# Kernel tuning notes

Hardware: AMD Instinct MI355X
Metric: run time of the kernel (lower is better)

The kernel has to match this reference:

```python
import jax, jax.numpy as jnp
import numpy as np

B, N, DIM = 8, 8192, 512
H, DH = 8, 64
INNER = H * DH
EPS = 1e-5


def setup_inputs() -> dict:
    key = jax.random.key(0)
    ks = jax.random.split(key, 5)
    x = jax.random.normal(ks[0], (B, N, DIM), dtype=jnp.float32)
    w_qkv = jax.random.normal(ks[1], (DIM, 3 * INNER), dtype=jnp.float32) * (DIM ** -0.5)
    ln_w = jnp.ones((INNER,), dtype=jnp.float32)
    ln_b = jnp.zeros((INNER,), dtype=jnp.float32)
    w_out = jax.random.normal(ks[2], (INNER, DIM), dtype=jnp.float32) * (INNER ** -0.5)
    b_out = jnp.zeros((DIM,), dtype=jnp.float32)
    return {"x": x, "w_qkv": w_qkv, "ln_w": ln_w, "ln_b": ln_b,
            "w_out": w_out, "b_out": b_out}


def _layernorm(x, w, b):
    mu = jnp.mean(x, axis=-1, keepdims=True)
    var = jnp.mean(jnp.square(x - mu), axis=-1, keepdims=True)
    return (x - mu) * jax.lax.rsqrt(var + EPS) * w + b


def reference(x, w_qkv, ln_w, ln_b, w_out, b_out):
    b, n, _ = x.shape
    qkv = x @ w_qkv  # [b, n, 3*inner]
    q, k, v = jnp.split(qkv, 3, axis=-1)
    # b n (h d) -> b h n d
    def heads(t):
        return t.reshape(b, n, H, DH).transpose(0, 2, 1, 3)
    q, k, v = heads(q), heads(k), heads(v)
    q = jax.nn.relu(q)
    k = jax.nn.relu(k)
    kv = jnp.einsum('bhnm,bhnd->bhmd', k, v)   # [b, h, d, d]
    out = jnp.einsum('bhnm,bhmd->bhnd', q, kv)  # [b, h, n, d]
    out = out.transpose(0, 2, 1, 3).reshape(b, n, INNER)
    out = _layernorm(out, ln_w, ln_b)
    return out @ w_out + b_out
```

## Files before the change

kernel.cpp:

```cpp
#include <hip/hip_runtime.h>
#include <stdint.h>

#define B_ 8
#define N_ 8192
#define DIM_ 512
#define H_ 8
#define DH_ 64
#define ROWS (B_*N_)
#define TRIPLE (3*DIM_)
#define EPS_ 1e-5f

typedef __attribute__((ext_vector_type(8))) short short8;
typedef __attribute__((ext_vector_type(4))) float f32x4;
typedef __attribute__((ext_vector_type(4))) float fl4;
typedef __attribute__((ext_vector_type(4))) unsigned short us4;
typedef __attribute__((ext_vector_type(8))) unsigned short us8;

#define AS1 __attribute__((address_space(1)))
#define AS3 __attribute__((address_space(3)))

__device__ __forceinline__ void gld16(const void* g, void* l) {
    __builtin_amdgcn_global_load_lds((const AS1 void*)(uintptr_t)g,
                                     (AS3 void*)(unsigned)(uintptr_t)l, 16, 0, 0);
}

__device__ inline unsigned short f2bf(float f) {
    union { float f; unsigned int u; } x; x.f = f;
    unsigned int r = x.u + 0x7fffu + ((x.u >> 16) & 1u);
    return (unsigned short)(r >> 16);
}
__device__ inline float bf2f(unsigned short b) {
    union { unsigned int u; float f; } x; x.u = ((unsigned int)b) << 16;
    return x.f;
}

__global__ __launch_bounds__(256) void k_cvt(const float* __restrict__ x,
                                             unsigned short* __restrict__ xb) {
    size_t i = ((size_t)blockIdx.x * 256 + threadIdx.x) * 8;
    fl4 a = *(const fl4*)(x + i);
    fl4 b = *(const fl4*)(x + i + 4);
    us8 r;
    r[0] = f2bf(a[0]); r[1] = f2bf(a[1]); r[2] = f2bf(a[2]); r[3] = f2bf(a[3]);
    r[4] = f2bf(b[0]); r[5] = f2bf(b[1]); r[6] = f2bf(b[2]); r[7] = f2bf(b[3]);
    *(us8*)(xb + i) = r;
}

__global__ void k_prep(const float* __restrict__ w_qkv, const float* __restrict__ w_out,
                       unsigned short* __restrict__ wqkvT, unsigned short* __restrict__ woutT) {
    int idx = blockIdx.x * 256 + threadIdx.x;
    if (idx < TRIPLE * DIM_) {
        int n = idx / DIM_, k = idx - n * DIM_;
        wqkvT[idx] = f2bf(w_qkv[(size_t)k * TRIPLE + n]);
    }
    if (idx < DIM_ * DIM_) {
        int n = idx / DIM_, k = idx - n * DIM_;
        woutT[idx] = f2bf(w_out[(size_t)k * DIM_ + n]);
    }
}

__global__ __launch_bounds__(256) void k_qkv_a(const unsigned short* __restrict__ xb,
        const unsigned short* __restrict__ wT,
        unsigned short* __restrict__ qkv)
{
    __shared__ unsigned short As[128 * 32];
    __shared__ unsigned short Bs[128 * 32];
    int t = threadIdx.x;
    int lane = t & 63, wave = t >> 6;
    int m0 = blockIdx.y * 128;
    int n0 = blockIdx.x * 128;
    int wm = (wave & 1) * 64, wn = (wave >> 1) * 64;
    int lr = lane & 15, kg = (lane >> 4) * 8;
    int srow = lane >> 2;
    int scol = (lane & 3) * 8;

    f32x4 acc[4][4] = {};
    for (int k0 = 0; k0 < DIM_; k0 += 32) {
#pragma unroll
        for (int i = 0; i < 2; ++i) {
            int c = wave * 2 + i;
            int r = c * 16 + srow;
            gld16(xb + (size_t)(m0 + r) * DIM_ + k0 + scol, &As[c * 512]);
            gld16(wT + (size_t)(n0 + r) * DIM_ + k0 + scol, &Bs[c * 512]);
        }
        __syncthreads();
        short8 af[4], bfr[4];
#pragma unroll
        for (int i = 0; i < 4; ++i) af[i]  = *(short8*)&As[(wm + i*16 + lr) * 32 + kg];
#pragma unroll
        for (int j = 0; j < 4; ++j) bfr[j] = *(short8*)&Bs[(wn + j*16 + lr) * 32 + kg];
#pragma unroll
        for (int i = 0; i < 4; ++i)
#pragma unroll
            for (int j = 0; j < 4; ++j)
                acc[i][j] = __builtin_amdgcn_mfma_f32_16x16x32_bf16(af[i], bfr[j], acc[i][j], 0, 0, 0);
        __syncthreads();
    }
#pragma unroll
    for (int i = 0; i < 4; ++i) {
        int row = m0 + wm + i*16 + (lane >> 4) * 4;
#pragma unroll
        for (int j = 0; j < 4; ++j) {
            int col = n0 + wn + j*16 + (lane & 15);
            bool rl = (col < 1024);
#pragma unroll
            for (int r = 0; r < 4; ++r) {
                float v = acc[i][j][r];
                if (rl && v < 0.0f) v = 0.0f;
                qkv[(size_t)(row + r) * TRIPLE + col] = f2bf(v);
            }
        }
    }
}

__global__ __launch_bounds__(256) void k_qkv_f(const float* __restrict__ x,
        const unsigned short* __restrict__ wT,
        unsigned short* __restrict__ qkv)
{
    __shared__ unsigned short As[128][40];
    __shared__ unsigned short Bs[128][40];
    int t = threadIdx.x;
    int lane = t & 63, wave = t >> 6;
    int m0 = blockIdx.y * 128;
    int n0 = blockIdx.x * 128;
    int wm = (wave & 1) * 64, wn = (wave >> 1) * 64;
    int lr = lane & 15, kg = (lane >> 4) * 8;

    f32x4 acc[4][4] = {};
    for (int k0 = 0; k0 < DIM_; k0 += 32) {
#pragma unroll
        for (int i = 0; i < 4; ++i) {
            int c = t + 256 * i;
            int r = c >> 3, c4 = (c & 7) * 4;
            fl4 v = *(const fl4*)(x + (size_t)(m0 + r) * DIM_ + k0 + c4);
            unsigned short* dst = &As[r][c4];
            dst[0] = f2bf(v[0]); dst[1] = f2bf(v[1]); dst[2] = f2bf(v[2]); dst[3] = f2bf(v[3]);
        }
#pragma unroll
        for (int i = 0; i < 2; ++i) {
            int c = t + 256 * i;
            int r = c >> 2, c8 = (c & 3) * 8;
            *(int4*)&Bs[r][c8] = *(const int4*)(wT + (size_t)(n0 + r) * DIM_ + k0 + c8);
        }
        __syncthreads();
        short8 af[4], bfr[4];
#pragma unroll
        for (int i = 0; i < 4; ++i) af[i]  = *(short8*)&As[wm + i*16 + lr][kg];
#pragma unroll
        for (int j = 0; j < 4; ++j) bfr[j] = *(short8*)&Bs[wn + j*16 + lr][kg];
#pragma unroll
        for (int i = 0; i < 4; ++i)
#pragma unroll
            for (int j = 0; j < 4; ++j)
                acc[i][j] = __builtin_amdgcn_mfma_f32_16x16x32_bf16(af[i], bfr[j], acc[i][j], 0, 0, 0);
        __syncthreads();
    }
#pragma unroll
    for (int i = 0; i < 4; ++i) {
        int row = m0 + wm + i*16 + (lane >> 4) * 4;
#pragma unroll
        for (int j = 0; j < 4; ++j) {
            int col = n0 + wn + j*16 + (lane & 15);
            bool rl = (col < 1024);
#pragma unroll
            for (int r = 0; r < 4; ++r) {
                float v = acc[i][j][r];
                if (rl && v < 0.0f) v = 0.0f;
                qkv[(size_t)(row + r) * TRIPLE + col] = f2bf(v);
            }
        }
    }
}

__global__ __launch_bounds__(256) void k_kv(const unsigned short* __restrict__ qkv,
                                            float* __restrict__ kv)
{
    __shared__ unsigned short KT[64][136];
    __shared__ unsigned short VT[64][136];
    __shared__ float red[64 * 64];
    int t = threadIdx.x, lane = t & 63, wave = t >> 6;
    int bh = blockIdx.x;
    int b = bh >> 3, h = bh & 7;
    int chunk = blockIdx.y;
    size_t rowbase = (size_t)b * N_ + (size_t)chunk * 1024;
    int kcol = DIM_ + h * 64;
    int vcol = 2 * DIM_ + h * 64;
    int lr = lane & 15;

    f32x4 acc[4][4] = {};
    for (int tile = 0; tile < 8; ++tile) {
        size_t r0 = rowbase + tile * 128;
#pragma unroll
        for (int i = 0; i < 8; ++i) {
            int c = t + 256 * i;
            int r = c >> 4, f4 = (c & 15) * 4;
            us4 kq = *(const us4*)(qkv + (r0 + r) * TRIPLE + kcol + f4);
            us4 vq = *(const us4*)(qkv + (r0 + r) * TRIPLE + vcol + f4);
#pragma unroll
            for (int j = 0; j < 4; ++j) { KT[f4 + j][r] = kq[j]; VT[f4 + j][r] = vq[j]; }
        }
        __syncthreads();
        int kg = wave * 32 + (lane >> 4) * 8;
        short8 af[4], bfr[4];
#pragma unroll
        for (int i = 0; i < 4; ++i) af[i]  = *(short8*)&KT[i*16 + lr][kg];
#pragma unroll
        for (int j = 0; j < 4; ++j) bfr[j] = *(short8*)&VT[j*16 + lr][kg];
#pragma unroll
        for (int i = 0; i < 4; ++i)
#pragma unroll
            for (int j = 0; j < 4; ++j)
                acc[i][j] = __builtin_amdgcn_mfma_f32_16x16x32_bf16(af[i], bfr[j], acc[i][j], 0, 0, 0);
        __syncthreads();
    }
    for (int w = 0; w < 4; ++w) {
        if (wave == w) {
#pragma unroll
            for (int i = 0; i < 4; ++i)
#pragma unroll
                for (int j = 0; j < 4; ++j)
#pragma unroll
                    for (int r = 0; r < 4; ++r) {
                        int m = i*16 + (lane >> 4) * 4 + r;
                        int d = j*16 + (lane & 15);
                        if (w == 0) red[m * 64 + d] = acc[i][j][r];
                        else        red[m * 64 + d] += acc[i][j][r];
                    }
        }
        __syncthreads();
    }
    float* kvout = kv + (size_t)bh * 4096;
#pragma unroll
    for (int i = 0; i < 16; ++i) {
        int idx = t + 256 * i;
        atomicAdd(&kvout[idx], red[idx]);
    }
}

__global__ __launch_bounds__(256) void k_attn(unsigned short* __restrict__ qkv,
                                              const float* __restrict__ kv)
{
    __shared__ unsigned short Qh[128][72];
    __shared__ unsigned short kvT[64][72];
    int t = threadIdx.x, lane = t & 63, wave = t >> 6;
    size_t r0 = (size_t)blockIdx.x * 128;
    int b = (int)(r0 / N_);
    int lr = lane & 15;
    for (int h = 0; h < H_; ++h) {
#pragma unroll
        for (int i = 0; i < 8; ++i) {
            int c = t + 256 * i;
            int r = c >> 4, f4 = (c & 15) * 4;
            *(us4*)&Qh[r][f4] = *(const us4*)(qkv + (r0 + r) * TRIPLE + h * 64 + f4);
        }
        const float* kvh = kv + (size_t)(b * 8 + h) * 4096;
#pragma unroll
        for (int i = 0; i < 16; ++i) {
            int idx = t + 256 * i;
            int m = idx >> 6, d = idx & 63;
            kvT[d][m] = f2bf(kvh[idx]);
        }
        __syncthreads();
        f32x4 acc[2][4] = {};
#pragma unroll
        for (int ks = 0; ks < 2; ++ks) {
            int kg = ks * 32 + (lane >> 4) * 8;
            short8 af[2], bfr[4];
#pragma unroll
            for (int i = 0; i < 2; ++i) af[i]  = *(short8*)&Qh[wave*32 + i*16 + lr][kg];
#pragma unroll
            for (int j = 0; j < 4; ++j) bfr[j] = *(short8*)&kvT[j*16 + lr][kg];
#pragma unroll
            for (int i = 0; i < 2; ++i)
#pragma unroll
                for (int j = 0; j < 4; ++j)
                    acc[i][j] = __builtin_amdgcn_mfma_f32_16x16x32_bf16(af[i], bfr[j], acc[i][j], 0, 0, 0);
        }
        __syncthreads();
#pragma unroll
        for (int i = 0; i < 2; ++i)
#pragma unroll
            for (int j = 0; j < 4; ++j) {
                int row = wave*32 + i*16 + (lane >> 4) * 4;
                int col = h*64 + j*16 + (lane & 15);
#pragma unroll
                for (int r = 0; r < 4; ++r)
                    qkv[(r0 + row + r) * TRIPLE + col] = f2bf(acc[i][j][r]);
            }
    }
}

__global__ __launch_bounds__(256) void k_out(const unsigned short* __restrict__ qkv,
        const unsigned short* __restrict__ woutT,
        const float* __restrict__ lnw, const float* __restrict__ lnb,
        const float* __restrict__ bout, float* __restrict__ out)
{
    __shared__ unsigned short As[128][40];
    __shared__ unsigned short Bs[128][40];
    __shared__ float mu[128], rs[128], lw[512], lb[512];
    int t = threadIdx.x, lane = t & 63, wave = t >> 6;
    int m0 = blockIdx.y * 128, n0 = blockIdx.x * 128;
    int wm = (wave & 1) * 64, wn = (wave >> 1) * 64;
    int lr = lane & 15, kg = (lane >> 4) * 8;

    for (int i = t; i < 512; i += 256) { lw[i] = lnw[i]; lb[i] = lnb[i]; }
    {
        int row = t >> 1, half = t & 1;
        const unsigned short* p = qkv + (size_t)(m0 + row) * TRIPLE + half * 256;
        float s = 0.0f, ss = 0.0f;
#pragma unroll 8
        for (int i = 0; i < 64; ++i) {
            us4 v = *(const us4*)(p + i * 4);
#pragma unroll
            for (int j = 0; j < 4; ++j) { float f = bf2f(v[j]); s += f; ss += f * f; }
        }
        s  += __shfl_xor(s, 1);
        ss += __shfl_xor(ss, 1);
        if (half == 0) {
            float m = s * (1.0f / 512.0f);
            float var = ss * (1.0f / 512.0f) - m * m;
            mu[row] = m;
            rs[row] = rsqrtf(var + EPS_);
        }
    }
    __syncthreads();

    f32x4 acc[4][4] = {};
    for (int k0 = 0; k0 < 512; k0 += 32) {
#pragma unroll
        for (int i = 0; i < 4; ++i) {
            int c = t + 256 * i;
            int r = c >> 3, c4 = (c & 7) * 4;
            us4 v = *(const us4*)(qkv + (size_t)(m0 + r) * TRIPLE + k0 + c4);
            float mm = mu[r], rr = rs[r];
            unsigned short* dst = &As[r][c4];
#pragma unroll
            for (int j = 0; j < 4; ++j) {
                float f = (bf2f(v[j]) - mm) * rr * lw[k0 + c4 + j] + lb[k0 + c4 + j];
                dst[j] = f2bf(f);
            }
        }
#pragma unroll
        for (int i = 0; i < 2; ++i) {
            int c = t + 256 * i;
            int r = c >> 2, c8 = (c & 3) * 8;
            *(int4*)&Bs[r][c8] = *(const int4*)(woutT + (size_t)(n0 + r) * DIM_ + k0 + c8);
        }
        __syncthreads();
        short8 af[4], bfr[4];
#pragma unroll
        for (int i = 0; i < 4; ++i) af[i]  = *(short8*)&As[wm + i*16 + lr][kg];
#pragma unroll
        for (int j = 0; j < 4; ++j) bfr[j] = *(short8*)&Bs[wn + j*16 + lr][kg];
#pragma unroll
        for (int i = 0; i < 4; ++i)
#pragma unroll
            for (int j = 0; j < 4; ++j)
                acc[i][j] = __builtin_amdgcn_mfma_f32_16x16x32_bf16(af[i], bfr[j], acc[i][j], 0, 0, 0);
        __syncthreads();
    }
#pragma unroll
    for (int i = 0; i < 4; ++i) {
        int row = m0 + wm + i*16 + (lane >> 4) * 4;
#pragma unroll
        for (int j = 0; j < 4; ++j) {
            int col = n0 + wn + j*16 + (lane & 15);
            float bo = bout[col];
#pragma unroll
            for (int r = 0; r < 4; ++r)
                out[(size_t)(row + r) * DIM_ + col] = acc[i][j][r] + bo;
        }
    }
}

extern "C" void kernel_launch(void* const* d_in, const int* in_sizes, int n_in,
                              void* d_out, int out_size, void* d_ws, size_t ws_size,
                              hipStream_t stream) {
    (void)in_sizes; (void)n_in; (void)out_size;
    const float* x     = (const float*)d_in[0];
    const float* w_qkv = (const float*)d_in[1];
    const float* ln_w  = (const float*)d_in[2];
    const float* ln_b  = (const float*)d_in[3];
    const float* w_out = (const float*)d_in[4];
    const float* b_out = (const float*)d_in[5];
    float* out = (float*)d_out;

    char* ws = (char*)d_ws;
    const size_t QKV_BYTES = (size_t)ROWS * TRIPLE * sizeof(unsigned short);
    const size_t KV_BYTES  = (size_t)64 * 64 * 64 * sizeof(float);
    const size_t WQT_BYTES = (size_t)TRIPLE * DIM_ * sizeof(unsigned short);
    const size_t WOT_BYTES = (size_t)DIM_ * DIM_ * sizeof(unsigned short);
    const size_t XB_BYTES  = (size_t)ROWS * DIM_ * sizeof(unsigned short);
    unsigned short* qkv   = (unsigned short*)ws;
    float*          kvbuf = (float*)(ws + QKV_BYTES);
    unsigned short* wqkvT = (unsigned short*)(ws + QKV_BYTES + KV_BYTES);
    unsigned short* woutT = (unsigned short*)(ws + QKV_BYTES + KV_BYTES + WQT_BYTES);
    unsigned short* xb    = (unsigned short*)(ws + QKV_BYTES + KV_BYTES + WQT_BYTES + WOT_BYTES);
    const size_t NEED = QKV_BYTES + KV_BYTES + WQT_BYTES + WOT_BYTES + XB_BYTES;

    hipMemsetAsync(kvbuf, 0, KV_BYTES, stream);
    k_prep<<<3072, 256, 0, stream>>>(w_qkv, w_out, wqkvT, woutT);
    if (ws_size >= NEED) {
        k_cvt<<<16384, 256, 0, stream>>>(x, xb);
        k_qkv_a<<<dim3(12, 512), 256, 0, stream>>>(xb, wqkvT, qkv);
    } else {
        k_qkv_f<<<dim3(12, 512), 256, 0, stream>>>(x, wqkvT, qkv);
    }
    k_kv<<<dim3(64, 8), 256, 0, stream>>>(qkv, kvbuf);
    k_attn<<<512, 256, 0, stream>>>(qkv, kvbuf);
    k_out<<<dim3(4, 512), 256, 0, stream>>>(qkv, woutT, ln_w, ln_b, b_out, out);
}
```

Before: 570.8 us.

## Rewrite QKV GEMM as 256x256 tile, double-buffered, 8-wave pingpong kernel

```diff
diff --git a/kernel.cpp b/kernel.cpp
--- a/kernel.cpp
+++ b/kernel.cpp
@@ -58,53 +58,146 @@
     }
 }
 
-__global__ __launch_bounds__(256) void k_qkv_a(const unsigned short* __restrict__ xb,
+__global__ __launch_bounds__(512, 2) void k_qkv8(const unsigned short* __restrict__ xb,
         const unsigned short* __restrict__ wT,
         unsigned short* __restrict__ qkv)
 {
-    __shared__ unsigned short As[128 * 32];
-    __shared__ unsigned short Bs[128 * 32];
-    int t = threadIdx.x;
-    int lane = t & 63, wave = t >> 6;
-    int m0 = blockIdx.y * 128;
-    int n0 = blockIdx.x * 128;
-    int wm = (wave & 1) * 64, wn = (wave >> 1) * 64;
-    int lr = lane & 15, kg = (lane >> 4) * 8;
-    int srow = lane >> 2;
-    int scol = (lane & 3) * 8;
-
-    f32x4 acc[4][4] = {};
-    for (int k0 = 0; k0 < DIM_; k0 += 32) {
-#pragma unroll
-        for (int i = 0; i < 2; ++i) {
-            int c = wave * 2 + i;
-            int r = c * 16 + srow;
-            gld16(xb + (size_t)(m0 + r) * DIM_ + k0 + scol, &As[c * 512]);
-            gld16(wT + (size_t)(n0 + r) * DIM_ + k0 + scol, &Bs[c * 512]);
-        }
-        __syncthreads();
-        short8 af[4], bfr[4];
-#pragma unroll
-        for (int i = 0; i < 4; ++i) af[i]  = *(short8*)&As[(wm + i*16 + lr) * 32 + kg];
-#pragma unroll
-        for (int j = 0; j < 4; ++j) bfr[j] = *(short8*)&Bs[(wn + j*16 + lr) * 32 + kg];
-#pragma unroll
-        for (int i = 0; i < 4; ++i)
-#pragma unroll
-            for (int j = 0; j < 4; ++j)
-                acc[i][j] = __builtin_amdgcn_mfma_f32_16x16x32_bf16(af[i], bfr[j], acc[i][j], 0, 0, 0);
-        __syncthreads();
-    }
-#pragma unroll
-    for (int i = 0; i < 4; ++i) {
-        int row = m0 + wm + i*16 + (lane >> 4) * 4;
+    __shared__ __align__(1024) unsigned short Ab[2][16384];
+    __shared__ __align__(1024) unsigned short Bb[2][16384];
+
+    const int tid  = threadIdx.x;
+    const int lane = tid & 63;
+    const int wid  = tid >> 6;
+    const int wr   = wid >> 2;
+    const int wc   = wid & 3;
+    const int lr   = lane & 15;
+
+    int id  = blockIdx.x;
+    int nid = (id & 7) * 192 + (id >> 3);
+    int n0  = (nid % 6) * 256;
+    int m0  = (nid / 6) * 256;
+
+    const unsigned short* pA[4];
+    const unsigned short* pB[4];
+    unsigned ldst[4];
+#pragma unroll
+    for (int j = 0; j < 4; ++j) {
+        int s    = tid + j * 512;
+        int row  = ((s >> 7) << 4) + ((s >> 2) & 15);
+        int colb = ((s & 3) << 4) ^ (((s >> 5) & 1) << 5);
+        int col  = ((s >> 6) & 1) * 32 + (colb >> 1);
+        pA[j] = xb + (size_t)(m0 + row) * 512 + col;
+        pB[j] = wT + (size_t)(n0 + row) * 512 + col;
+        ldst[j] = (unsigned)((j * 512 + wid * 64) * 8);
+    }
+    const int lo = lr * 32 + ((((lane >> 4) << 4) ^ ((lr >> 3) << 5)) >> 1);
+
+    auto STAGE = [&](int t, int c) {
 #pragma unroll
         for (int j = 0; j < 4; ++j) {
-            int col = n0 + wn + j*16 + (lane & 15);
+            gld16(pA[j] + t * 64, (void*)&Ab[c][ldst[j]]);
+            gld16(pB[j] + t * 64, (void*)&Bb[c][ldst[j]]);
+        }
+    };
+
+    f32x4 acc[8][4] = {};
+    short8 af[4][2], bf0[2][2], bf1[2][2];
+
+    STAGE(0, 0);
+    asm volatile("s_waitcnt vmcnt(0)" ::: "memory");
+    __builtin_amdgcn_s_barrier();
+
+    for (int t = 0; t < 8; ++t) {
+        const int cur = t & 1;
+        const unsigned short* Ac = Ab[cur];
+        const unsigned short* Bc = Bb[cur];
+
+        if (t < 7) STAGE(t + 1, cur ^ 1);
+#pragma unroll
+        for (int m = 0; m < 4; ++m)
+#pragma unroll
+            for (int ks = 0; ks < 2; ++ks)
+                af[m][ks] = *(const short8*)&Ac[(wr * 16 + m * 2 + ks) * 512 + lo];
+#pragma unroll
+        for (int n = 0; n < 2; ++n)
+#pragma unroll
+            for (int ks = 0; ks < 2; ++ks)
+                bf0[n][ks] = *(const short8*)&Bc[((wc * 4 + n) * 2 + ks) * 512 + lo];
+        __builtin_amdgcn_s_barrier();
+        __builtin_amdgcn_s_setprio(1);
+#pragma unroll
+        for (int m = 0; m < 4; ++m)
+#pragma unroll
+            for (int n = 0; n < 2; ++n)
+#pragma unroll
+                for (int ks = 0; ks < 2; ++ks)
+                    acc[m][n] = __builtin_amdgcn_mfma_f32_16x16x32_bf16(af[m][ks], bf0[n][ks], acc[m][n], 0, 0, 0);
+        __builtin_amdgcn_s_setprio(0);
+        __builtin_amdgcn_s_barrier();
+
+#pragma unroll
+        for (int n = 0; n < 2; ++n)
+#pragma unroll
+            for (int ks = 0; ks < 2; ++ks)
+                bf1[n][ks] = *(const short8*)&Bc[((wc * 4 + 2 + n) * 2 + ks) * 512 + lo];
+        __builtin_amdgcn_s_barrier();
+        __builtin_amdgcn_s_setprio(1);
+#pragma unroll
+        for (int m = 0; m < 4; ++m)
+#pragma unroll
+            for (int n = 0; n < 2; ++n)
+#pragma unroll
+                for (int ks = 0; ks < 2; ++ks)
+                    acc[m][2 + n] = __builtin_amdgcn_mfma_f32_16x16x32_bf16(af[m][ks], bf1[n][ks], acc[m][2 + n], 0, 0, 0);
+        __builtin_amdgcn_s_setprio(0);
+        __builtin_amdgcn_s_barrier();
+
+#pragma unroll
+        for (int m = 0; m < 4; ++m)
+#pragma unroll
+            for (int ks = 0; ks < 2; ++ks)
+                af[m][ks] = *(const short8*)&Ac[(wr * 16 + (4 + m) * 2 + ks) * 512 + lo];
+        __builtin_amdgcn_s_barrier();
+        __builtin_amdgcn_s_setprio(1);
+#pragma unroll
+        for (int m = 0; m < 4; ++m)
+#pragma unroll
+            for (int n = 0; n < 2; ++n)
+#pragma unroll
+                for (int ks = 0; ks < 2; ++ks)
+                    acc[4 + m][2 + n] = __builtin_amdgcn_mfma_f32_16x16x32_bf16(af[m][ks], bf1[n][ks], acc[4 + m][2 + n], 0, 0, 0);
+        __builtin_amdgcn_s_setprio(0);
+        __builtin_amdgcn_s_barrier();
+
+#pragma unroll
+        for (int n = 0; n < 2; ++n)
+#pragma unroll
+            for (int ks = 0; ks < 2; ++ks)
+                bf0[n][ks] = *(const short8*)&Bc[((wc * 4 + n) * 2 + ks) * 512 + lo];
+        __builtin_amdgcn_s_barrier();
+        __builtin_amdgcn_s_setprio(1);
+#pragma unroll
+        for (int m = 0; m < 4; ++m)
+#pragma unroll
+            for (int n = 0; n < 2; ++n)
+#pragma unroll
+                for (int ks = 0; ks < 2; ++ks)
+                    acc[4 + m][n] = __builtin_amdgcn_mfma_f32_16x16x32_bf16(af[m][ks], bf0[n][ks], acc[4 + m][n], 0, 0, 0);
+        __builtin_amdgcn_s_setprio(0);
+        if (t < 7) asm volatile("s_waitcnt vmcnt(0)" ::: "memory");
+        __builtin_amdgcn_s_barrier();
+    }
+
+#pragma unroll
+    for (int m = 0; m < 8; ++m) {
+        int row = m0 + wr * 128 + m * 16 + ((lane >> 4) << 2);
+#pragma unroll
+        for (int n = 0; n < 4; ++n) {
+            int col = n0 + wc * 64 + n * 16 + (lane & 15);
             bool rl = (col < 1024);
 #pragma unroll
             for (int r = 0; r < 4; ++r) {
-                float v = acc[i][j][r];
+                float v = acc[m][n][r];
                 if (rl && v < 0.0f) v = 0.0f;
                 qkv[(size_t)(row + r) * TRIPLE + col] = f2bf(v);
             }
@@ -401,7 +494,7 @@
     k_prep<<<3072, 256, 0, stream>>>(w_qkv, w_out, wqkvT, woutT);
     if (ws_size >= NEED) {
         k_cvt<<<16384, 256, 0, stream>>>(x, xb);
-        k_qkv_a<<<dim3(12, 512), 256, 0, stream>>>(xb, wqkvT, qkv);
+        k_qkv8<<<dim3(1536), 512, 0, stream>>>(xb, wqkvT, qkv);
     } else {
         k_qkv_f<<<dim3(12, 512), 256, 0, stream>>>(x, wqkvT, qkv);
     }
```

Measured after the change: 569.3 us. About the same (-0.3%).
